# Performance work log

Hardware: AMD Instinct MI355X
Metric: run time of the kernel (lower is better)

Reference implementation:

```python
import jax, jax.numpy as jnp
import numpy as np

BATCH, D_INNER, DT_RANK, N = 256, 5120, 160, 16

def _softplus_thresh(z, threshold=20.0):
    # softplus(z) with beta=1; linear above threshold (matches ttnn.softplus(parameter1=1, parameter2=20))
    return jnp.where(z > threshold, z, jax.nn.softplus(z))

def setup_inputs() -> dict:
    key = jax.random.key(0)
    ks = jax.random.split(key, 9)
    s = lambda d: 1.0 / np.sqrt(d)
    return {
        "x": jax.random.normal(ks[0], (1, 1, BATCH, D_INNER), jnp.float32),
        "h": jax.random.normal(ks[1], (BATCH, D_INNER, N), jnp.float32) * 0.1,
        "W_delta": jax.random.normal(ks[2], (D_INNER, DT_RANK), jnp.float32) * s(D_INNER),
        "W_dt": jax.random.normal(ks[3], (DT_RANK, D_INNER), jnp.float32) * s(DT_RANK),
        "b_dt": jax.random.normal(ks[4], (D_INNER,), jnp.float32) * 0.1,
        "A_log": jax.random.uniform(ks[5], (D_INNER, N), jnp.float32, 0.0, 1.5),
        "W_B": jax.random.normal(ks[6], (D_INNER, N), jnp.float32) * s(D_INNER),
        "W_C": jax.random.normal(ks[7], (D_INNER, N), jnp.float32) * s(D_INNER),
        "D": jax.random.normal(ks[8], (D_INNER,), jnp.float32),
    }

def reference(x, h, W_delta, W_dt, b_dt, A_log, W_B, W_C, D):
    # x: (1,1,B,d_inner) single decode step; h: (B,d_inner,n) SSM state
    xb = x.reshape(BATCH, D_INNER)                           # (B, d)
    # delta = softplus(x @ W_delta @ W_dt + b_dt)           -> (B, d)
    dt = _softplus_thresh((xb @ W_delta) @ W_dt + b_dt)
    A = -jnp.exp(A_log)                                      # (d, n)
    abar = jnp.exp(dt[:, :, None] * A[None, :, :])           # (B, d, n)
    Bp = xb @ W_B                                            # (B, n)
    # bbar * x: delta * B * x, broadcast over state dim
    bx = (dt * xb)[:, :, None] * Bp[:, None, :]              # (B, d, n)
    h_new = abar * h + bx                                    # (B, d, n) new hidden state
    C = xb @ W_C                                             # (B, n)
    y = jnp.einsum("bdn,bn->bd", h_new, C) + xb * D          # readout + skip (D)
    return y.reshape(1, 1, BATCH, D_INNER)
```

## Files before the change

kernel.cpp:

```cpp
#include <hip/hip_runtime.h>
#include <math.h>

#define BATCH 256
#define DIN   5120
#define RANK  160
#define NS    16
#define NCAT  192

__global__ __launch_bounds__(256) void k1_gemm(
    const float* __restrict__ x, const float* __restrict__ Wd,
    const float* __restrict__ WB, const float* __restrict__ WC,
    float* __restrict__ P, float* __restrict__ Bp, float* __restrict__ Cc)
{
    __shared__ float xT[32][64];
    __shared__ float Wt[32][64];
    const int t  = threadIdx.x;
    const int m0 = blockIdx.x * 64;
    const int n0 = blockIdx.y * 64;
    const int k0 = blockIdx.z * 256;
    const int tm = (t >> 4) * 4;
    const int tn = (t & 15) * 4;

    const int lm  = t >> 2;
    const int lk  = (t & 3) * 8;
    const int ln  = t & 63;
    const int lkb = (t >> 6) * 8;

    const float* wsrc; int wstr;
    {
        const int c = n0 + ln;
        if (c < RANK)            { wsrc = Wd + c;                wstr = RANK; }
        else if (c < RANK + NS)  { wsrc = WB + (c - RANK);       wstr = NS;   }
        else                     { wsrc = WC + (c - RANK - NS);  wstr = NS;   }
    }

    float acc[4][4] = {{0.f}};

    for (int ks = 0; ks < 8; ++ks) {
        const int kb = k0 + ks * 32;
        {
            const float* src = x + (size_t)(m0 + lm) * DIN + kb + lk;
            const float4 a0 = *(const float4*)src;
            const float4 a1 = *(const float4*)(src + 4);
            xT[lk+0][lm]=a0.x; xT[lk+1][lm]=a0.y; xT[lk+2][lm]=a0.z; xT[lk+3][lm]=a0.w;
            xT[lk+4][lm]=a1.x; xT[lk+5][lm]=a1.y; xT[lk+6][lm]=a1.z; xT[lk+7][lm]=a1.w;
        }
        {
            const float* wp = wsrc + (size_t)(kb + lkb) * wstr;
            #pragma unroll
            for (int i = 0; i < 8; ++i) { Wt[lkb + i][ln] = *wp; wp += wstr; }
        }
        __syncthreads();
        #pragma unroll
        for (int k = 0; k < 32; ++k) {
            const float4 a = *(const float4*)&xT[k][tm];
            const float4 b = *(const float4*)&Wt[k][tn];
            acc[0][0] += a.x*b.x; acc[0][1] += a.x*b.y; acc[0][2] += a.x*b.z; acc[0][3] += a.x*b.w;
            acc[1][0] += a.y*b.x; acc[1][1] += a.y*b.y; acc[1][2] += a.y*b.z; acc[1][3] += a.y*b.w;
            acc[2][0] += a.z*b.x; acc[2][1] += a.z*b.y; acc[2][2] += a.z*b.z; acc[2][3] += a.z*b.w;
            acc[3][0] += a.w*b.x; acc[3][1] += a.w*b.y; acc[3][2] += a.w*b.z; acc[3][3] += a.w*b.w;
        }
        __syncthreads();
    }

    #pragma unroll
    for (int i = 0; i < 4; ++i) {
        const int gm = m0 + tm + i;
        #pragma unroll
        for (int j = 0; j < 4; ++j) {
            const int c = n0 + tn + j;
            float* dst;
            if (c < RANK)           dst = P  + gm * RANK + c;
            else if (c < RANK + NS) dst = Bp + gm * NS + (c - RANK);
            else                    dst = Cc + gm * NS + (c - RANK - NS);
            atomicAdd(dst, acc[i][j]);
        }
    }
}

__device__ __forceinline__ float softplus20(float z)
{
    if (z > 20.f) return z;
    return fmaxf(z, 0.f) + log1pf(__expf(-fabsf(z)));
}

__global__ __launch_bounds__(256) void k2_gemm(
    const float* __restrict__ P, const float* __restrict__ Wdt,
    const float* __restrict__ bdt, float* __restrict__ dtb)
{
    __shared__ float aT[32][64];
    __shared__ float Bt[32][64];
    const int t  = threadIdx.x;
    const int m0 = blockIdx.x * 64;
    const int n0 = blockIdx.y * 64;
    const int tm = (t >> 4) * 4;
    const int tn = (t & 15) * 4;

    const int lm  = t >> 2;
    const int lk  = (t & 3) * 8;
    const int ln  = t & 63;
    const int lkb = (t >> 6) * 8;

    float acc[4][4] = {{0.f}};

    for (int ks = 0; ks < 5; ++ks) {
        const int kb = ks * 32;
        {
            const float* src = P + (size_t)(m0 + lm) * RANK + kb + lk;
            const float4 a0 = *(const float4*)src;
            const float4 a1 = *(const float4*)(src + 4);
            aT[lk+0][lm]=a0.x; aT[lk+1][lm]=a0.y; aT[lk+2][lm]=a0.z; aT[lk+3][lm]=a0.w;
            aT[lk+4][lm]=a1.x; aT[lk+5][lm]=a1.y; aT[lk+6][lm]=a1.z; aT[lk+7][lm]=a1.w;
        }
        {
            const float* wp = Wdt + (size_t)(kb + lkb) * DIN + n0 + ln;
            #pragma unroll
            for (int i = 0; i < 8; ++i) { Bt[lkb + i][ln] = wp[(size_t)i * DIN]; }
        }
        __syncthreads();
        #pragma unroll
        for (int k = 0; k < 32; ++k) {
            const float4 a = *(const float4*)&aT[k][tm];
            const float4 b = *(const float4*)&Bt[k][tn];
            acc[0][0] += a.x*b.x; acc[0][1] += a.x*b.y; acc[0][2] += a.x*b.z; acc[0][3] += a.x*b.w;
            acc[1][0] += a.y*b.x; acc[1][1] += a.y*b.y; acc[1][2] += a.y*b.z; acc[1][3] += a.y*b.w;
            acc[2][0] += a.z*b.x; acc[2][1] += a.z*b.y; acc[2][2] += a.z*b.z; acc[2][3] += a.z*b.w;
            acc[3][0] += a.w*b.x; acc[3][1] += a.w*b.y; acc[3][2] += a.w*b.z; acc[3][3] += a.w*b.w;
        }
        __syncthreads();
    }

    const float4 bz = *(const float4*)&bdt[n0 + tn];
    #pragma unroll
    for (int i = 0; i < 4; ++i) {
        const int gm = m0 + tm + i;
        float4 o;
        o.x = softplus20(acc[i][0] + bz.x);
        o.y = softplus20(acc[i][1] + bz.y);
        o.z = softplus20(acc[i][2] + bz.z);
        o.w = softplus20(acc[i][3] + bz.w);
        *(float4*)&dtb[(size_t)gm * DIN + n0 + tn] = o;
    }
}

__global__ __launch_bounds__(256) void k3_ssm(
    const float* __restrict__ x, const float* __restrict__ h,
    const float* __restrict__ A_log, const float* __restrict__ dtb,
    const float* __restrict__ Bp, const float* __restrict__ Cc,
    const float* __restrict__ Dv, float* __restrict__ y)
{
    __shared__ float sB[NS], sC[NS];
    const int b = blockIdx.x / 20;
    const int d = (blockIdx.x % 20) * 256 + threadIdx.x;
    if (threadIdx.x < NS)            sB[threadIdx.x]      = Bp[b * NS + threadIdx.x];
    else if (threadIdx.x < 2 * NS)   sC[threadIdx.x - NS] = Cc[b * NS + threadIdx.x - NS];
    __syncthreads();

    const float dtv = dtb[(size_t)b * DIN + d];
    const float xv  = x[(size_t)b * DIN + d];
    const float dtx = dtv * xv;
    const float4* hp = (const float4*)(h + ((size_t)b * DIN + d) * NS);
    const float4* ap = (const float4*)(A_log + (size_t)d * NS);

    float acc = 0.f;
    #pragma unroll
    for (int q = 0; q < 4; ++q) {
        const float4 h4 = hp[q];
        const float4 a4 = ap[q];
        const float ab0 = __expf(dtv * -__expf(a4.x));
        const float ab1 = __expf(dtv * -__expf(a4.y));
        const float ab2 = __expf(dtv * -__expf(a4.z));
        const float ab3 = __expf(dtv * -__expf(a4.w));
        acc += (ab0 * h4.x + dtx * sB[4*q+0]) * sC[4*q+0];
        acc += (ab1 * h4.y + dtx * sB[4*q+1]) * sC[4*q+1];
        acc += (ab2 * h4.z + dtx * sB[4*q+2]) * sC[4*q+2];
        acc += (ab3 * h4.w + dtx * sB[4*q+3]) * sC[4*q+3];
    }
    y[(size_t)b * DIN + d] = acc + xv * Dv[d];
}

extern "C" void kernel_launch(void* const* d_in, const int* in_sizes, int n_in,
                              void* d_out, int out_size, void* d_ws, size_t ws_size,
                              hipStream_t stream)
{
    const float* x     = (const float*)d_in[0];
    const float* h     = (const float*)d_in[1];
    const float* Wd    = (const float*)d_in[2];
    const float* Wdt   = (const float*)d_in[3];
    const float* bdt   = (const float*)d_in[4];
    const float* A_log = (const float*)d_in[5];
    const float* WB    = (const float*)d_in[6];
    const float* WC    = (const float*)d_in[7];
    const float* Dv    = (const float*)d_in[8];
    float* out = (float*)d_out;

    float* ws  = (float*)d_ws;
    float* P   = ws;
    float* Bp  = ws + BATCH * RANK;
    float* Cc  = Bp + BATCH * NS;
    float* dtb = Cc + BATCH * NS;

    hipMemsetAsync(ws, 0, (size_t)BATCH * NCAT * sizeof(float), stream);

    k1_gemm<<<dim3(4, 3, 20), 256, 0, stream>>>(x, Wd, WB, WC, P, Bp, Cc);
    k2_gemm<<<dim3(4, 80),    256, 0, stream>>>(P, Wdt, bdt, dtb);
    k3_ssm <<<dim3(BATCH * 20), 256, 0, stream>>>(x, h, A_log, dtb, Bp, Cc, Dv, out);
}
```

Before: 197.9 us.

## Fuse dt projection GEMM with SSM update, four batch rows per block

The second GEMM (P @ W_dt + bias, softplus) is merged into the SSM kernel, so dt is computed in registers and no longer round-trips through a global workspace buffer. Each block handles 256 channels for 4 batch rows. It reads each W_dt column once per 4 rows and reuses the precomputed -exp(A_log) across those rows. The cost is that W_dt is re-read from global or L2 by 64 row-groups, with an uncoalesced-free but non-tiled inner-product loop. The grid is also much smaller than the old per-(batch,chunk) grid, which may lower occupancy or latency hiding.

```diff
diff --git a/kernel.cpp b/kernel.cpp
--- a/kernel.cpp
+++ b/kernel.cpp
@@ -84,99 +84,77 @@
     return fmaxf(z, 0.f) + log1pf(__expf(-fabsf(z)));
 }
 
-__global__ __launch_bounds__(256) void k2_gemm(
+__global__ __launch_bounds__(256) void k2_fused(
     const float* __restrict__ P, const float* __restrict__ Wdt,
-    const float* __restrict__ bdt, float* __restrict__ dtb)
-{
-    __shared__ float aT[32][64];
-    __shared__ float Bt[32][64];
-    const int t  = threadIdx.x;
-    const int m0 = blockIdx.x * 64;
-    const int n0 = blockIdx.y * 64;
-    const int tm = (t >> 4) * 4;
-    const int tn = (t & 15) * 4;
-
-    const int lm  = t >> 2;
-    const int lk  = (t & 3) * 8;
-    const int ln  = t & 63;
-    const int lkb = (t >> 6) * 8;
-
-    float acc[4][4] = {{0.f}};
-
-    for (int ks = 0; ks < 5; ++ks) {
-        const int kb = ks * 32;
-        {
-            const float* src = P + (size_t)(m0 + lm) * RANK + kb + lk;
-            const float4 a0 = *(const float4*)src;
-            const float4 a1 = *(const float4*)(src + 4);
-            aT[lk+0][lm]=a0.x; aT[lk+1][lm]=a0.y; aT[lk+2][lm]=a0.z; aT[lk+3][lm]=a0.w;
-            aT[lk+4][lm]=a1.x; aT[lk+5][lm]=a1.y; aT[lk+6][lm]=a1.z; aT[lk+7][lm]=a1.w;
-        }
-        {
-            const float* wp = Wdt + (size_t)(kb + lkb) * DIN + n0 + ln;
-            #pragma unroll
-            for (int i = 0; i < 8; ++i) { Bt[lkb + i][ln] = wp[(size_t)i * DIN]; }
-        }
-        __syncthreads();
-        #pragma unroll
-        for (int k = 0; k < 32; ++k) {
-            const float4 a = *(const float4*)&aT[k][tm];
-            const float4 b = *(const float4*)&Bt[k][tn];
-            acc[0][0] += a.x*b.x; acc[0][1] += a.x*b.y; acc[0][2] += a.x*b.z; acc[0][3] += a.x*b.w;
-            acc[1][0] += a.y*b.x; acc[1][1] += a.y*b.y; acc[1][2] += a.y*b.z; acc[1][3] += a.y*b.w;
-            acc[2][0] += a.z*b.x; acc[2][1] += a.z*b.y; acc[2][2] += a.z*b.z; acc[2][3] += a.z*b.w;
-            acc[3][0] += a.w*b.x; acc[3][1] += a.w*b.y; acc[3][2] += a.w*b.z; acc[3][3] += a.w*b.w;
-        }
-        __syncthreads();
-    }
-
-    const float4 bz = *(const float4*)&bdt[n0 + tn];
-    #pragma unroll
-    for (int i = 0; i < 4; ++i) {
-        const int gm = m0 + tm + i;
-        float4 o;
-        o.x = softplus20(acc[i][0] + bz.x);
-        o.y = softplus20(acc[i][1] + bz.y);
-        o.z = softplus20(acc[i][2] + bz.z);
-        o.w = softplus20(acc[i][3] + bz.w);
-        *(float4*)&dtb[(size_t)gm * DIN + n0 + tn] = o;
-    }
-}
-
-__global__ __launch_bounds__(256) void k3_ssm(
-    const float* __restrict__ x, const float* __restrict__ h,
-    const float* __restrict__ A_log, const float* __restrict__ dtb,
+    const float* __restrict__ bdt, const float* __restrict__ x,
+    const float* __restrict__ h, const float* __restrict__ A_log,
     const float* __restrict__ Bp, const float* __restrict__ Cc,
     const float* __restrict__ Dv, float* __restrict__ y)
 {
-    __shared__ float sB[NS], sC[NS];
-    const int b = blockIdx.x / 20;
-    const int d = (blockIdx.x % 20) * 256 + threadIdx.x;
-    if (threadIdx.x < NS)            sB[threadIdx.x]      = Bp[b * NS + threadIdx.x];
-    else if (threadIdx.x < 2 * NS)   sC[threadIdx.x - NS] = Cc[b * NS + threadIdx.x - NS];
+    __shared__ float sP[4][RANK];
+    __shared__ float sB[4][NS];
+    __shared__ float sC[4][NS];
+
+    const int tid = threadIdx.x;
+    const int d   = blockIdx.x * 256 + tid;
+    const int b0  = blockIdx.y * 4;
+
+    #pragma unroll
+    for (int i = tid; i < 4 * RANK; i += 256)
+        sP[i / RANK][i % RANK] = P[(size_t)b0 * RANK + i];
+    if (tid < 64)                    sB[tid >> 4][tid & 15] = Bp[b0 * NS + tid];
+    else if (tid < 128) { int u = tid - 64; sC[u >> 4][u & 15] = Cc[b0 * NS + u]; }
     __syncthreads();
 
-    const float dtv = dtb[(size_t)b * DIN + d];
-    const float xv  = x[(size_t)b * DIN + d];
-    const float dtx = dtv * xv;
-    const float4* hp = (const float4*)(h + ((size_t)b * DIN + d) * NS);
-    const float4* ap = (const float4*)(A_log + (size_t)d * NS);
+    float acc0 = 0.f, acc1 = 0.f, acc2 = 0.f, acc3 = 0.f;
+    const float* wcol = Wdt + d;
+    #pragma unroll 8
+    for (int k = 0; k < RANK; ++k) {
+        const float w = wcol[(size_t)k * DIN];
+        acc0 += sP[0][k] * w;
+        acc1 += sP[1][k] * w;
+        acc2 += sP[2][k] * w;
+        acc3 += sP[3][k] * w;
+    }
+    const float bb = bdt[d];
+    float dt[4];
+    dt[0] = softplus20(acc0 + bb);
+    dt[1] = softplus20(acc1 + bb);
+    dt[2] = softplus20(acc2 + bb);
+    dt[3] = softplus20(acc3 + bb);
 
-    float acc = 0.f;
+    float A2[NS];
+    {
+        const float4* ap = (const float4*)(A_log + (size_t)d * NS);
+        #pragma unroll
+        for (int q = 0; q < 4; ++q) {
+            const float4 a4 = ap[q];
+            A2[4*q+0] = -__expf(a4.x);
+            A2[4*q+1] = -__expf(a4.y);
+            A2[4*q+2] = -__expf(a4.z);
+            A2[4*q+3] = -__expf(a4.w);
+        }
+    }
+    const float dv = Dv[d];
+
     #pragma unroll
-    for (int q = 0; q < 4; ++q) {
-        const float4 h4 = hp[q];
-        const float4 a4 = ap[q];
-        const float ab0 = __expf(dtv * -__expf(a4.x));
-        const float ab1 = __expf(dtv * -__expf(a4.y));
-        const float ab2 = __expf(dtv * -__expf(a4.z));
-        const float ab3 = __expf(dtv * -__expf(a4.w));
-        acc += (ab0 * h4.x + dtx * sB[4*q+0]) * sC[4*q+0];
-        acc += (ab1 * h4.y + dtx * sB[4*q+1]) * sC[4*q+1];
-        acc += (ab2 * h4.z + dtx * sB[4*q+2]) * sC[4*q+2];
-        acc += (ab3 * h4.w + dtx * sB[4*q+3]) * sC[4*q+3];
+    for (int b = 0; b < 4; ++b) {
+        const int gb = b0 + b;
+        const float dtv = dt[b];
+        const float xv  = x[(size_t)gb * DIN + d];
+        const float dtx = dtv * xv;
+        const float4* hp = (const float4*)(h + ((size_t)gb * DIN + d) * NS);
+        float acc = 0.f;
+        #pragma unroll
+        for (int q = 0; q < 4; ++q) {
+            const float4 h4 = hp[q];
+            acc += (__expf(dtv * A2[4*q+0]) * h4.x + dtx * sB[b][4*q+0]) * sC[b][4*q+0];
+            acc += (__expf(dtv * A2[4*q+1]) * h4.y + dtx * sB[b][4*q+1]) * sC[b][4*q+1];
+            acc += (__expf(dtv * A2[4*q+2]) * h4.z + dtx * sB[b][4*q+2]) * sC[b][4*q+2];
+            acc += (__expf(dtv * A2[4*q+3]) * h4.w + dtx * sB[b][4*q+3]) * sC[b][4*q+3];
+        }
+        y[(size_t)gb * DIN + d] = acc + xv * dv;
     }
-    y[(size_t)b * DIN + d] = acc + xv * Dv[d];
 }
 
 extern "C" void kernel_launch(void* const* d_in, const int* in_sizes, int n_in,
@@ -198,11 +176,9 @@
     float* P   = ws;
     float* Bp  = ws + BATCH * RANK;
     float* Cc  = Bp + BATCH * NS;
-    float* dtb = Cc + BATCH * NS;
 
     hipMemsetAsync(ws, 0, (size_t)BATCH * NCAT * sizeof(float), stream);
 
-    k1_gemm<<<dim3(4, 3, 20), 256, 0, stream>>>(x, Wd, WB, WC, P, Bp, Cc);
-    k2_gemm<<<dim3(4, 80),    256, 0, stream>>>(P, Wdt, bdt, dtb);
-    k3_ssm <<<dim3(BATCH * 20), 256, 0, stream>>>(x, h, A_log, dtb, Bp, Cc, Dv, out);
+    k1_gemm <<<dim3(4, 3, 20), 256, 0, stream>>>(x, Wd, WB, WC, P, Bp, Cc);
+    k2_fused<<<dim3(20, 64),   256, 0, stream>>>(P, Wdt, bdt, x, h, A_log, Bp, Cc, Dv, out);
 }
```

After: 190.1 us. 1.04x faster.
